# Optimization experiments

Measured on AMD Instinct MI355X. Metric: run time of the kernel, lower is better.

Reference implementation:

```python
import jax, jax.numpy as jnp
import numpy as np
from jax import lax

B = 1024          # batch
C = 64            # HSI channels (forced by reshape to [b,100,64,3,3])
HW = 11           # spatial size (forced by hard-coded output (b,100,11,11))
GEN_OUT = 6400    # ge_w out channels; 6400*3*3 == 100*64*3*3
EPS = 1e-5


def setup_inputs() -> dict:
    key = jax.random.key(0)
    k = jax.random.split(key, 6)
    x_in   = jax.random.normal(k[0], (B, C, HW, HW), dtype=jnp.float32)
    # Conv2d(2, 6400, (3,3), stride=4) weight [O, I, kh, kw] and bias [O]
    ge_w_w = jax.random.normal(k[1], (GEN_OUT, 2, 3, 3), dtype=jnp.float32) * 0.05
    ge_w_b = jax.random.normal(k[2], (GEN_OUT,), dtype=jnp.float32) * 0.01
    # BatchNorm2d(6400) parameters (eval mode: running stats)
    bn_gamma = jnp.ones((GEN_OUT,), dtype=jnp.float32)
    bn_beta  = jnp.zeros((GEN_OUT,), dtype=jnp.float32)
    bn_mean  = jax.random.normal(k[3], (GEN_OUT,), dtype=jnp.float32) * 0.1
    bn_var   = jax.random.uniform(k[4], (GEN_OUT,), dtype=jnp.float32, minval=0.5, maxval=1.5)
    return {"x_in": x_in, "ge_w_w": ge_w_w, "ge_w_b": ge_w_b,
            "bn_gamma": bn_gamma, "bn_beta": bn_beta,
            "bn_mean": bn_mean, "bn_var": bn_var}


def reference(x_in, ge_w_w, ge_w_b, bn_gamma, bn_beta, bn_mean, bn_var):
    b = x_in.shape[0]
    # Channel-pool attention map: [b, 2, 11, 11]
    x_avg = jnp.mean(x_in, axis=1, keepdims=True)
    x_max = jnp.max(x_in, axis=1, keepdims=True)
    x_H = jnp.concatenate([x_avg, x_max], axis=1)

    # Filter-generating conv: [b, 6400, 3, 3]
    w_H = lax.conv_general_dilated(
        x_H, ge_w_w, window_strides=(4, 4), padding='VALID',
        dimension_numbers=('NCHW', 'OIHW', 'NCHW'))
    w_H = w_H + ge_w_b[None, :, None, None]
    # BatchNorm2d (eval) + ReLU
    inv = bn_gamma / jnp.sqrt(bn_var + EPS)
    w_H = (w_H - bn_mean[None, :, None, None]) * inv[None, :, None, None] \
          + bn_beta[None, :, None, None]
    w_H = jax.nn.relu(w_H)

    # Per-sample dynamic filters: [b, 100, 64, 3, 3]
    w_H = w_H.reshape(b, 100, C, 3, 3)

    # Per-sample conv2d(padding=1), batched via vmap: [b, 100, 11, 11]
    def per_sample(x, w):
        # x: [64,11,11], w: [100,64,3,3]
        y = lax.conv_general_dilated(
            x[None], w, window_strides=(1, 1), padding=((1, 1), (1, 1)),
            dimension_numbers=('NCHW', 'OIHW', 'NCHW'))
        return y[0]

    outputs = jax.vmap(per_sample)(x_in, w_H)
    return outputs
```

## Files before the change

### kernel.cpp

```cpp
#include <hip/hip_runtime.h>
#include <hip/hip_bf16.h>

using bf16x8 = __attribute__((ext_vector_type(8))) short;
using f32x4  = __attribute__((ext_vector_type(4))) float;

constexpr int CH  = 64;
constexpr int HW  = 11;
constexpr int NP  = 121;
constexpr int PPW = 14;
constexpr int NROW = 182;
constexpr int ICL = 72;
constexpr int IMG_USH = NROW * ICL;
constexpr int IMG_I4  = IMG_USH / 8;
constexpr int IMG_P   = 13312;
constexpr int NSEG    = 26;
constexpr int NO  = 7168;
constexpr float EPS = 1e-5f;

__device__ __forceinline__ f32x4 MFMA(bf16x8 a, bf16x8 b, f32x4 c) {
    return __builtin_amdgcn_mfma_f32_16x16x32_bf16(a, b, c, 0, 0, 0);
}

__global__ __launch_bounds__(256) void prep_kernel(
    const float* __restrict__ gw, const float* __restrict__ gb,
    const float* __restrict__ bng, const float* __restrict__ bnb,
    const float* __restrict__ bnm, const float* __restrict__ bnv,
    unsigned short* __restrict__ Aprep, float* __restrict__ Beta)
{
    int o = blockIdx.x * 256 + threadIdx.x;
    if (o >= NO) return;
    float inv = 0.f, beta = 0.f;
    if (o < 6400) {
        inv  = bng[o] * rsqrtf(bnv[o] + EPS);
        beta = (gb[o] - bnm[o]) * inv + bnb[o];
    }
    Beta[o] = beta;
    int tile = o >> 4, lrow = o & 15;
    #pragma unroll
    for (int jg = 0; jg < 4; ++jg) {
        bf16x8 f;
        #pragma unroll
        for (int r = 0; r < 8; ++r) {
            int k = jg * 8 + r;
            float v = (o < 6400 && k < 18) ? gw[(size_t)o * 18 + k] * inv : 0.f;
            __hip_bfloat16 h = __float2bfloat16(v);
            f[r] = *(short*)&h;
        }
        ((bf16x8*)Aprep)[tile * 64 + jg * 16 + lrow] = f;
    }
}

__global__ __launch_bounds__(256) void pool_kernel(
    const float* __restrict__ x_in,
    unsigned short* __restrict__ img,
    unsigned short* __restrict__ Bg)
{
    __shared__ alignas(16) unsigned short xsT[IMG_USH];
    __shared__ float xh[2][128];
    __shared__ float xhp[2][2][128];

    const int phys = blockIdx.x;
    const int b = (phys & 7) * 128 + (phys >> 3);
    const int t = threadIdx.x, lane = t & 63, wave = t >> 6;
    const float* xb = x_in + (size_t)b * (CH * NP);
    unsigned short* ib = img + (size_t)b * IMG_P;

    for (int i = t; i < IMG_USH / 2; i += 256) ((unsigned int*)xsT)[i] = 0u;
    __syncthreads();

    {
        int p = (wave & 1) * 64 + lane, ich = wave >> 1;
        if (p < NP) {
            int pp = (p / HW + 1) * PPW + (p % HW + 1);
            float s = 0.f, m = -INFINITY;
            const float* xc = xb + (ich * 32) * NP + p;
            #pragma unroll 8
            for (int q = 0; q < 32; ++q) {
                float v = xc[q * NP];
                s += v; m = fmaxf(m, v);
                __hip_bfloat16 h = __float2bfloat16(v);
                xsT[pp * ICL + ich * 32 + q] = *(unsigned short*)&h;
            }
            xhp[ich][0][p] = s;
            xhp[ich][1][p] = m;
        }
    }
    __syncthreads();
    if (t < NP) {
        xh[0][t] = (xhp[0][0][t] + xhp[1][0][t]) * (1.f / 64.f);
        xh[1][t] = fmaxf(xhp[0][1][t], xhp[1][1][t]);
    }
    __syncthreads();

    for (int i = t; i < 512; i += 256) {
        int tap = i >> 5, k = i & 31;
        float val = 0.f;
        if (tap < 9 && k < 18) {
            int ci = k / 9, o9 = k - ci * 9, u = o9 / 3, v = o9 - u * 3;
            int kh = tap / 3, kw = tap - kh * 3;
            val = xh[ci][(4 * kh + u) * HW + (4 * kw + v)];
        }
        __hip_bfloat16 h = __float2bfloat16(val);
        Bg[b * 512 + i] = *(unsigned short*)&h;
    }

    for (int i = t; i < IMG_I4; i += 256)
        ((int4*)ib)[i] = ((const int4*)xsT)[i];
}

__global__ __launch_bounds__(512, 4) void hsi_main(
    const unsigned short* __restrict__ img,
    const unsigned short* __restrict__ Bg,
    const unsigned short* __restrict__ Aprep,
    const float* __restrict__ Beta,
    float* __restrict__ out)
{
    __shared__ alignas(16) unsigned short xs[IMG_P];
    __shared__ alignas(16) unsigned short strip[2][18 * 64 * 8];

    const int phys = blockIdx.x;
    const int L = (phys & 7) * 512 + (phys >> 3);
    const int b = L >> 2, d = L & 3;
    const int t = threadIdx.x;
    const int lane = t & 63, wave = t >> 6;
    const int lrow = lane & 15, jg = lane >> 4;
    const int cl = wave >> 2;
    const int chunk = d * 2 + cl;

    {
        const unsigned short* ib = img + (size_t)b * IMG_P;
        #pragma unroll
        for (int i = 0; i < 4; ++i) {
            int seg = wave + i * 8;
            if (seg < NSEG)
                __builtin_amdgcn_global_load_lds(
                    (const __attribute__((address_space(1))) void*)(ib + seg * 512 + lane * 8),
                    (__attribute__((address_space(3))) void*)(xs + seg * 512),
                    16, 0, 0);
        }
    }

    const bf16x8 Bgen = *(const bf16x8*)(Bg + b * 512 + lrow * 32 + jg * 8);

    unsigned short* sp = strip[cl];
    const int tl0 = (wave & 3) * 14;
    #pragma unroll
    for (int bat = 0; bat < 2; ++bat) {
        bf16x8 Ar[7];
        float4 Br[7];
        #pragma unroll
        for (int j = 0; j < 7; ++j) {
            int tG = chunk * 56 + tl0 + bat * 7 + j;
            Ar[j] = *(const bf16x8*)(Aprep + ((size_t)tG * 64 + lane) * 8);
            Br[j] = *(const float4*)(Beta + (size_t)tG * 16 + jg * 4);
        }
        #pragma unroll
        for (int j = 0; j < 7; ++j) {
            int tl = tl0 + bat * 7 + j;
            f32x4 acc{};
            acc = MFMA(Ar[j], Bgen, acc);
            if (lrow < 9) {
                float v0 = fmaxf(acc[0] + Br[j].x, 0.f);
                float v1 = fmaxf(acc[1] + Br[j].y, 0.f);
                float v2 = fmaxf(acc[2] + Br[j].z, 0.f);
                float v3 = fmaxf(acc[3] + Br[j].w, 0.f);
                __hip_bfloat162 p01 = __float22bfloat162_rn(make_float2(v0, v1));
                __hip_bfloat162 p23 = __float22bfloat162_rn(make_float2(v2, v3));
                uint2 pk;
                pk.x = *(unsigned int*)&p01;
                pk.y = *(unsigned int*)&p23;
                int oc_l = tl >> 2, icb = tl & 3;
                int h   = icb >> 1;
                int jgr = (icb & 1) * 2 + (jg >> 1);
                int slot = (jgr * 16 + oc_l) ^ lrow;
                *(uint2*)(sp + ((lrow * 2 + h) * 64 + slot) * 8 + (jg & 1) * 4) = pk;
            }
        }
    }

    __syncthreads();

    int p0 = (wave & 3) * 32 + lrow;
    int p1 = p0 + 16;
    int pc0 = p0 > 120 ? 120 : p0;
    int pc1 = p1 > 120 ? 120 : p1;
    int base0 = (pc0 / HW) * PPW + (pc0 % HW);
    int base1 = (pc1 / HW) * PPW + (pc1 % HW);

    const char* spb = (const char*)sp;
    const int laneb = lane * 16;
    const char* xb0 = (const char*)xs + base0 * (ICL * 2) + jg * 16;
    const char* xb1 = (const char*)xs + base1 * (ICL * 2) + jg * 16;

    f32x4 acc0{}, acc1{};
    #pragma unroll
    for (int tap = 0; tap < 9; ++tap) {
        const int av   = laneb ^ (tap * 16);
        const int boff = ((tap / 3) * PPW + (tap % 3)) * (ICL * 2);
        #pragma unroll
        for (int h = 0; h < 2; ++h) {
            bf16x8 Af = *(const bf16x8*)(spb + (tap * 2 + h) * 1024 + av);
            bf16x8 B0 = *(const bf16x8*)(xb0 + boff + h * 64);
            bf16x8 B1 = *(const bf16x8*)(xb1 + boff + h * 64);
            acc0 = MFMA(Af, B0, acc0);
            acc1 = MFMA(Af, B1, acc1);
        }
    }

    float* ob = out + (size_t)b * 100 * NP;
    #pragma unroll
    for (int ri = 0; ri < 4; ++ri) {
        int row = jg * 4 + ri;
        int oc = chunk * 14 + row;
        if (row < 14 && oc < 100) {
            if (p0 < NP) ob[oc * NP + p0] = acc0[ri];
            if (p1 < NP) ob[oc * NP + p1] = acc1[ri];
        }
    }
}

extern "C" void kernel_launch(void* const* d_in, const int* in_sizes, int n_in,
                              void* d_out, int out_size, void* d_ws, size_t ws_size,
                              hipStream_t stream) {
    const float* x  = (const float*)d_in[0];
    const float* gw = (const float*)d_in[1];
    const float* gb = (const float*)d_in[2];
    const float* bg = (const float*)d_in[3];
    const float* bb = (const float*)d_in[4];
    const float* bm = (const float*)d_in[5];
    const float* bv = (const float*)d_in[6];
    float* out = (float*)d_out;

    unsigned short* Aprep = (unsigned short*)d_ws;
    float* Beta = (float*)((char*)d_ws + 458752);
    unsigned short* Bgm = (unsigned short*)((char*)d_ws + 487424);
    unsigned short* img = (unsigned short*)((char*)d_ws + 1536000);

    prep_kernel<<<NO / 256, 256, 0, stream>>>(gw, gb, bg, bb, bm, bv, Aprep, Beta);
    pool_kernel<<<1024, 256, 0, stream>>>(x, img, Bgm);
    hsi_main<<<1024 * 4, 512, 0, stream>>>(img, Bgm, Aprep, Beta, out);
}
```

Baseline: 76.67 us.

## Fold weight prep into pool kernel and reuse image fragments across both strips

The separate prep kernel is merged into the pool kernel: each of the 1024 blocks prepares 7 output channels' scaled weights and bias, which removes one kernel launch. In the main conv, each wave now covers 16 pixels for both 14-channel strips. It loads its 18 image B-fragments into registers once and reuses them across two strip passes, instead of each half-block computing 32 pixels for its own strip. This cuts LDS image reads but raises register pressure with 18 held fragments, and output stores are now split across two passes.

Result: faster. 67.14 us (-12.4%).

```diff
diff --git a/kernel.cpp b/kernel.cpp
--- a/kernel.cpp
+++ b/kernel.cpp
@@ -21,39 +21,14 @@
     return __builtin_amdgcn_mfma_f32_16x16x32_bf16(a, b, c, 0, 0, 0);
 }
 
-__global__ __launch_bounds__(256) void prep_kernel(
+__global__ __launch_bounds__(256) void pool_kernel(
+    const float* __restrict__ x_in,
     const float* __restrict__ gw, const float* __restrict__ gb,
     const float* __restrict__ bng, const float* __restrict__ bnb,
     const float* __restrict__ bnm, const float* __restrict__ bnv,
+    unsigned short* __restrict__ img,
+    unsigned short* __restrict__ Bg,
     unsigned short* __restrict__ Aprep, float* __restrict__ Beta)
-{
-    int o = blockIdx.x * 256 + threadIdx.x;
-    if (o >= NO) return;
-    float inv = 0.f, beta = 0.f;
-    if (o < 6400) {
-        inv  = bng[o] * rsqrtf(bnv[o] + EPS);
-        beta = (gb[o] - bnm[o]) * inv + bnb[o];
-    }
-    Beta[o] = beta;
-    int tile = o >> 4, lrow = o & 15;
-    #pragma unroll
-    for (int jg = 0; jg < 4; ++jg) {
-        bf16x8 f;
-        #pragma unroll
-        for (int r = 0; r < 8; ++r) {
-            int k = jg * 8 + r;
-            float v = (o < 6400 && k < 18) ? gw[(size_t)o * 18 + k] * inv : 0.f;
-            __hip_bfloat16 h = __float2bfloat16(v);
-            f[r] = *(short*)&h;
-        }
-        ((bf16x8*)Aprep)[tile * 64 + jg * 16 + lrow] = f;
-    }
-}
-
-__global__ __launch_bounds__(256) void pool_kernel(
-    const float* __restrict__ x_in,
-    unsigned short* __restrict__ img,
-    unsigned short* __restrict__ Bg)
 {
     __shared__ alignas(16) unsigned short xsT[IMG_USH];
     __shared__ float xh[2][128];
@@ -64,6 +39,27 @@
     const int t = threadIdx.x, lane = t & 63, wave = t >> 6;
     const float* xb = x_in + (size_t)b * (CH * NP);
     unsigned short* ib = img + (size_t)b * IMG_P;
+
+    if (t < 28) {
+        int o = phys * 7 + (t >> 2);
+        int jgp = t & 3;
+        float inv = 0.f, beta = 0.f;
+        if (o < 6400) {
+            inv  = bng[o] * rsqrtf(bnv[o] + EPS);
+            beta = (gb[o] - bnm[o]) * inv + bnb[o];
+        }
+        if (jgp == 0) Beta[o] = beta;
+        int tile = o >> 4, lr = o & 15;
+        bf16x8 f;
+        #pragma unroll
+        for (int r = 0; r < 8; ++r) {
+            int k = jgp * 8 + r;
+            float v = (o < 6400 && k < 18) ? gw[(size_t)o * 18 + k] * inv : 0.f;
+            __hip_bfloat16 h = __float2bfloat16(v);
+            f[r] = *(short*)&h;
+        }
+        ((bf16x8*)Aprep)[tile * 64 + jgp * 16 + lr] = f;
+    }
 
     for (int i = t; i < IMG_USH / 2; i += 256) ((unsigned int*)xsT)[i] = 0u;
     __syncthreads();
@@ -124,8 +120,6 @@
     const int t = threadIdx.x;
     const int lane = t & 63, wave = t >> 6;
     const int lrow = lane & 15, jg = lane >> 4;
-    const int cl = wave >> 2;
-    const int chunk = d * 2 + cl;
 
     {
         const unsigned short* ib = img + (size_t)b * IMG_P;
@@ -142,6 +136,8 @@
 
     const bf16x8 Bgen = *(const bf16x8*)(Bg + b * 512 + lrow * 32 + jg * 8);
 
+    const int cl = wave >> 2;
+    const int genchunk = d * 2 + cl;
     unsigned short* sp = strip[cl];
     const int tl0 = (wave & 3) * 14;
     #pragma unroll
@@ -150,7 +146,7 @@
         float4 Br[7];
         #pragma unroll
         for (int j = 0; j < 7; ++j) {
-            int tG = chunk * 56 + tl0 + bat * 7 + j;
+            int tG = genchunk * 56 + tl0 + bat * 7 + j;
             Ar[j] = *(const bf16x8*)(Aprep + ((size_t)tG * 64 + lane) * 8);
             Br[j] = *(const float4*)(Beta + (size_t)tG * 16 + jg * 4);
         }
@@ -180,41 +176,39 @@
 
     __syncthreads();
 
-    int p0 = (wave & 3) * 32 + lrow;
-    int p1 = p0 + 16;
-    int pc0 = p0 > 120 ? 120 : p0;
-    int pc1 = p1 > 120 ? 120 : p1;
-    int base0 = (pc0 / HW) * PPW + (pc0 % HW);
-    int base1 = (pc1 / HW) * PPW + (pc1 % HW);
-
-    const char* spb = (const char*)sp;
-    const int laneb = lane * 16;
-    const char* xb0 = (const char*)xs + base0 * (ICL * 2) + jg * 16;
-    const char* xb1 = (const char*)xs + base1 * (ICL * 2) + jg * 16;
-
-    f32x4 acc0{}, acc1{};
+    const int p  = wave * 16 + lrow;
+    const int pc = p > 120 ? 120 : p;
+    const int base = (pc / HW) * PPW + (pc % HW);
+    const char* xbp = (const char*)xs + base * (ICL * 2) + jg * 16;
+    bf16x8 Bf[18];
     #pragma unroll
     for (int tap = 0; tap < 9; ++tap) {
-        const int av   = laneb ^ (tap * 16);
         const int boff = ((tap / 3) * PPW + (tap % 3)) * (ICL * 2);
-        #pragma unroll
-        for (int h = 0; h < 2; ++h) {
-            bf16x8 Af = *(const bf16x8*)(spb + (tap * 2 + h) * 1024 + av);
-            bf16x8 B0 = *(const bf16x8*)(xb0 + boff + h * 64);
-            bf16x8 B1 = *(const bf16x8*)(xb1 + boff + h * 64);
-            acc0 = MFMA(Af, B0, acc0);
-            acc1 = MFMA(Af, B1, acc1);
-        }
+        Bf[tap * 2 + 0] = *(const bf16x8*)(xbp + boff);
+        Bf[tap * 2 + 1] = *(const bf16x8*)(xbp + boff + 64);
     }
 
     float* ob = out + (size_t)b * 100 * NP;
+    const int laneb = lane * 16;
     #pragma unroll
-    for (int ri = 0; ri < 4; ++ri) {
-        int row = jg * 4 + ri;
-        int oc = chunk * 14 + row;
-        if (row < 14 && oc < 100) {
-            if (p0 < NP) ob[oc * NP + p0] = acc0[ri];
-            if (p1 < NP) ob[oc * NP + p1] = acc1[ri];
+    for (int q = 0; q < 2; ++q) {
+        const char* spb = (const char*)strip[q];
+        const int chunk = d * 2 + q;
+        f32x4 acc{};
+        #pragma unroll
+        for (int tap = 0; tap < 9; ++tap) {
+            const int av = laneb ^ (tap * 16);
+            #pragma unroll
+            for (int h = 0; h < 2; ++h) {
+                bf16x8 Af = *(const bf16x8*)(spb + (tap * 2 + h) * 1024 + av);
+                acc = MFMA(Af, Bf[tap * 2 + h], acc);
+            }
+        }
+        #pragma unroll
+        for (int ri = 0; ri < 4; ++ri) {
+            int row = jg * 4 + ri;
+            int oc = chunk * 14 + row;
+            if (row < 14 && oc < 100 && p < NP) ob[oc * NP + p] = acc[ri];
         }
     }
 }
@@ -236,7 +230,7 @@
     unsigned short* Bgm = (unsigned short*)((char*)d_ws + 487424);
     unsigned short* img = (unsigned short*)((char*)d_ws + 1536000);
 
-    prep_kernel<<<NO / 256, 256, 0, stream>>>(gw, gb, bg, bb, bm, bv, Aprep, Beta);
-    pool_kernel<<<1024, 256, 0, stream>>>(x, img, Bgm);
+    pool_kernel<<<1024, 256, 0, stream>>>(x, gw, gb, bg, bb, bm, bv,
+                                          img, Bgm, Aprep, Beta);
     hsi_main<<<1024 * 4, 512, 0, stream>>>(img, Bgm, Aprep, Beta, out);
 }
```
